# Kernel tuning notes

Measured on AMD Instinct MI355X. Metric: run time of the kernel, lower is better.

The kernel has to match this reference:

```python
import jax, jax.numpy as jnp
import numpy as np

V, N, K, D = 100000, 20000, 32, 128
NEG = -1e9  # masked logit value


def setup_inputs() -> dict:
    key = jax.random.key(0)
    ks = jax.random.split(key, 8)
    return {
        "nodes": jax.random.randint(ks[0], (N,), 0, V),
        "neigh_idx": jax.random.randint(ks[1], (N, K), 0, V),
        "degrees": jax.random.randint(ks[2], (N,), 0, K + 1),
        "u2e": jax.random.normal(ks[3], (V, D), dtype=jnp.float32),
        "W1": jax.random.normal(ks[4], (2 * D, D), dtype=jnp.float32) * 0.05,
        "b1": jnp.zeros((D,), jnp.float32),
        "W2": jax.random.normal(ks[5], (D, D), dtype=jnp.float32) * 0.05,
        "b2": jnp.zeros((D,), jnp.float32),
        "W3": jax.random.normal(ks[6], (D, 1), dtype=jnp.float32) * 0.05,
        "b3": jnp.zeros((1,), jnp.float32),
    }


def reference(nodes, neigh_idx, degrees, u2e, W1, b1, W2, b2, W3, b3):
    self_feats = u2e[nodes]                      # [N, D]
    e_u = u2e[neigh_idx]                         # [N, K, D] ragged gather (padded)
    # Attention MLP: cat(neighbor, self) -> relu -> relu -> scalar logit
    x = jnp.concatenate([e_u, jnp.broadcast_to(self_feats[:, None, :], (e_u.shape[0], K, D))], axis=-1)  # [N, K, 2D]
    h = jax.nn.relu(x @ W1 + b1)                 # [N, K, D]
    h = jax.nn.relu(h @ W2 + b2)                 # [N, K, D]
    logits = (h @ W3 + b3)[..., 0]               # [N, K]
    mask = jnp.arange(K)[None, :] < degrees[:, None]
    att = jax.nn.softmax(jnp.where(mask, logits, NEG), axis=-1)  # softmax over neighbors
    agg = jnp.einsum("nk,nkd->nd", att, e_u)     # attention-weighted neighbor sum
    out = jnp.where(degrees[:, None] > 0, (agg + self_feats) * 0.5, self_feats)
    return out
```

## Files before the change

kernel.cpp:

```cpp
#include <hip/hip_runtime.h>
#include <hip/hip_bf16.h>

#define KK 32
#define DD 128
#define NEGV (-1e9f)
#define SE 136
#define PREP_BLKS 2048

typedef __attribute__((ext_vector_type(8))) short bf16x8;
typedef __attribute__((ext_vector_type(4))) float f32x4;

__device__ __forceinline__ unsigned short f2bf(float f) {
    union { float f; unsigned u; } v; v.f = f;
    unsigned r = v.u + 0x7fffu + ((v.u >> 16) & 1u);
    return (unsigned short)(r >> 16);
}
__device__ __forceinline__ float bf2f(unsigned short h) {
    union { unsigned u; float f; } v; v.u = ((unsigned)h) << 16;
    return v.f;
}
__device__ __forceinline__ unsigned pk2(float x, float y) {
    union { __hip_bfloat162 h; unsigned u; } c;
    c.h = __float22bfloat162_rn(float2{x, y});
    return c.u;
}

__global__ __launch_bounds__(256) void prep_kernel(
    const float* __restrict__ u2e, const float* __restrict__ W1, const float* __restrict__ W2,
    unsigned short* __restrict__ u2e_bf, unsigned short* __restrict__ W1t,
    unsigned short* __restrict__ W2t, const int u2e_blocks, const long Vd)
{
    const int b = blockIdx.x;
    if (b < u2e_blocks) {
        const long stride = (long)u2e_blocks * 256 * 8;
        for (long i = ((long)b * 256 + threadIdx.x) * 8; i < Vd; i += stride) {
            const float4 v0 = *(const float4*)(u2e + i);
            const float4 v1 = *(const float4*)(u2e + i + 4);
            uint4 p;
            p.x = pk2(v0.x, v0.y); p.y = pk2(v0.z, v0.w);
            p.z = pk2(v1.x, v1.y); p.w = pk2(v1.z, v1.w);
            *(uint4*)(u2e_bf + i) = p;
        }
    } else {
        const int id = (b - u2e_blocks) * 256 + threadIdx.x;
        if (id < 256 * 128) {
            const int n = id >> 8, k = id & 255;
            W1t[id] = f2bf(W1[k * DD + n]);
        } else {
            const int j = id - 256 * 128;
            const int n = j >> 7, k = j & 127;
            W2t[j] = f2bf(W2[k * DD + n]);
        }
    }
}

template<bool BF>
__global__ __launch_bounds__(256, 2) void ppagg_mfma(
    const int* __restrict__ nodes, const int* __restrict__ neigh,
    const int* __restrict__ degrees, const float* __restrict__ u2e,
    const unsigned short* __restrict__ u2e_bf,
    const unsigned short* __restrict__ W1t, const unsigned short* __restrict__ W2t,
    const float* __restrict__ b1, const float* __restrict__ b2,
    const float* __restrict__ W3, const float* __restrict__ b3,
    float* __restrict__ out, const int Nn)
{
    __shared__ __align__(16) unsigned short s_A[128 * SE];
    __shared__ __align__(16) unsigned short s_B[128 * SE];
    __shared__ __align__(16) unsigned short s_x8[8 * DD];
    __shared__ float s_selfc[8 * 128];
    __shared__ float s_part[4][128];

    const int tid  = threadIdx.x;
    const int w    = tid >> 6;
    const int lane = tid & 63;
    const int ln   = lane & 15;
    const int q    = lane >> 4;

    const int nb = blockIdx.x * 8;
    const int r  = tid & 127;
    const int h  = tid >> 7;

    int idxA, idxB, vA, vB;
    {
        int ng0 = nb + (r >> 5);       if (ng0 >= Nn) ng0 = Nn - 1;
        int ng1 = nb + 4 + (r >> 5);   if (ng1 >= Nn) ng1 = Nn - 1;
        idxA = neigh[ng0 * KK + (r & 31)];
        idxB = neigh[ng1 * KK + (r & 31)];
        vA = (r & 31) < degrees[ng0];
        vB = (r & 31) < degrees[ng1];
    }

    auto stage = [&](unsigned short* buf, int idx, int v) {
        unsigned short* dst = buf + r * SE + h * 64;
        if (BF && v) {
            const uint4* src = (const uint4*)(u2e_bf + (long)idx * DD + h * 64);
            #pragma unroll
            for (int c = 0; c < 8; ++c) *(uint4*)(dst + c * 8) = src[c];
        } else if (!BF && v) {
            const float4* src = (const float4*)(u2e + (long)idx * DD + h * 64);
            #pragma unroll
            for (int c8 = 0; c8 < 8; ++c8) {
                const float4 v0 = src[c8 * 2];
                const float4 v1 = src[c8 * 2 + 1];
                uint4 p;
                p.x = pk2(v0.x, v0.y); p.y = pk2(v0.z, v0.w);
                p.z = pk2(v1.x, v1.y); p.w = pk2(v1.z, v1.w);
                *(uint4*)(dst + c8 * 8) = p;
            }
        } else {
            const uint4 z = {0u, 0u, 0u, 0u};
            #pragma unroll
            for (int c = 0; c < 8; ++c) *(uint4*)(dst + c * 8) = z;
        }
    };

    stage(s_A, idxA, vA);

    {
        int gn = nb + (tid >> 5); if (gn >= Nn) gn = Nn - 1;
        const int g = tid >> 5, p = tid & 31;
        const float4 v = *(const float4*)(u2e + (long)nodes[gn] * DD + p * 4);
        *(unsigned*)(s_x8 + g * DD + p * 4)     = pk2(v.x, v.y);
        *(unsigned*)(s_x8 + g * DD + p * 4 + 2) = pk2(v.z, v.w);
    }

    float2 self0, self1;
    {
        int n0 = nb + w;       if (n0 >= Nn) n0 = Nn - 1;
        int n1 = nb + 4 + w;   if (n1 >= Nn) n1 = Nn - 1;
        self0 = *(const float2*)(u2e + (long)nodes[n0] * DD + lane * 2);
        self1 = *(const float2*)(u2e + (long)nodes[n1] * DD + lane * 2);
    }

    bf16x8 b1f[4][2], b2f[4][2];
    float b1c[2], b2c[2], w3c[2];
    const int c0 = w * 32 + ln;
    const int c1 = c0 + 16;
    #pragma unroll
    for (int kk = 0; kk < 4; ++kk) {
        b1f[kk][0] = *(const bf16x8*)(W1t + c0 * 256 + kk * 32 + q * 8);
        b1f[kk][1] = *(const bf16x8*)(W1t + c1 * 256 + kk * 32 + q * 8);
        b2f[kk][0] = *(const bf16x8*)(W2t + c0 * 128 + kk * 32 + q * 8);
        b2f[kk][1] = *(const bf16x8*)(W2t + c1 * 128 + kk * 32 + q * 8);
    }
    b1c[0] = b1[c0]; b1c[1] = b1[c1];
    b2c[0] = b2[c0]; b2c[1] = b2[c1];
    w3c[0] = W3[c0]; w3c[1] = W3[c1];
    const float b3v = b3[0];

    __syncthreads();

    {
        f32x4 a0 = (f32x4){0.f,0.f,0.f,0.f}, a1 = (f32x4){0.f,0.f,0.f,0.f};
        #pragma unroll
        for (int kk = 0; kk < 4; ++kk) {
            const bf16x8 av = *(const bf16x8*)(s_x8 + (ln & 7) * DD + kk * 32 + q * 8);
            const bf16x8 w0 = *(const bf16x8*)(W1t + c0 * 256 + 128 + kk * 32 + q * 8);
            const bf16x8 w1 = *(const bf16x8*)(W1t + c1 * 256 + 128 + kk * 32 + q * 8);
            a0 = __builtin_amdgcn_mfma_f32_16x16x32_bf16(av, w0, a0, 0, 0, 0);
            a1 = __builtin_amdgcn_mfma_f32_16x16x32_bf16(av, w1, a1, 0, 0, 0);
        }
        if (q < 2) {
            #pragma unroll
            for (int rr = 0; rr < 4; ++rr) {
                s_selfc[(q * 4 + rr) * 128 + c0] = a0[rr] + b1c[0];
                s_selfc[(q * 4 + rr) * 128 + c1] = a1[rr] + b1c[1];
            }
        }
    }
    __syncthreads();

    #pragma unroll
    for (int it = 0; it < 2; ++it) {
        unsigned short* E = it ? s_B : s_A;
        unsigned short* H = it ? s_A : s_B;
        const int gbase = nb + it * 4;
        const float2 selfv = it ? self1 : self0;

        if (it == 1) __syncthreads();

        f32x4 acc[8][2];
        #pragma unroll
        for (int mt = 0; mt < 8; ++mt) {
            acc[mt][0] = (f32x4){0.f, 0.f, 0.f, 0.f};
            acc[mt][1] = (f32x4){0.f, 0.f, 0.f, 0.f};
        }
        #pragma unroll
        for (int kk = 0; kk < 4; ++kk) {
            bf16x8 a[8];
            #pragma unroll
            for (int mt = 0; mt < 8; ++mt)
                a[mt] = *(const bf16x8*)(E + (mt * 16 + ln) * SE + kk * 32 + q * 8);
            #pragma unroll
            for (int mt = 0; mt < 8; ++mt) {
                acc[mt][0] = __builtin_amdgcn_mfma_f32_16x16x32_bf16(a[mt], b1f[kk][0], acc[mt][0], 0, 0, 0);
                acc[mt][1] = __builtin_amdgcn_mfma_f32_16x16x32_bf16(a[mt], b1f[kk][1], acc[mt][1], 0, 0, 0);
            }
        }
        #pragma unroll
        for (int mt = 0; mt < 8; ++mt) {
            const float sc0 = s_selfc[(it * 4 + (mt >> 1)) * 128 + c0];
            const float sc1 = s_selfc[(it * 4 + (mt >> 1)) * 128 + c1];
            #pragma unroll
            for (int rr = 0; rr < 4; rr += 2) {
                const int row = mt * 16 + q * 4 + rr;
                const unsigned p0 = pk2(fmaxf(acc[mt][0][rr]     + sc0, 0.f),
                                        fmaxf(acc[mt][0][rr + 1] + sc0, 0.f));
                const unsigned p1v = pk2(fmaxf(acc[mt][1][rr]     + sc1, 0.f),
                                         fmaxf(acc[mt][1][rr + 1] + sc1, 0.f));
                H[row * SE + c0]       = (unsigned short)(p0 & 0xffffu);
                H[(row + 1) * SE + c0] = (unsigned short)(p0 >> 16);
                H[row * SE + c1]       = (unsigned short)(p1v & 0xffffu);
                H[(row + 1) * SE + c1] = (unsigned short)(p1v >> 16);
            }
        }
        __syncthreads();

        f32x4 acc2[8][2];
        #pragma unroll
        for (int mt = 0; mt < 8; ++mt) {
            acc2[mt][0] = (f32x4){0.f, 0.f, 0.f, 0.f};
            acc2[mt][1] = (f32x4){0.f, 0.f, 0.f, 0.f};
        }
        #pragma unroll
        for (int kk = 0; kk < 4; ++kk) {
            bf16x8 a[8];
            #pragma unroll
            for (int mt = 0; mt < 8; ++mt)
                a[mt] = *(const bf16x8*)(H + (mt * 16 + ln) * SE + kk * 32 + q * 8);
            #pragma unroll
            for (int mt = 0; mt < 8; ++mt) {
                acc2[mt][0] = __builtin_amdgcn_mfma_f32_16x16x32_bf16(a[mt], b2f[kk][0], acc2[mt][0], 0, 0, 0);
                acc2[mt][1] = __builtin_amdgcn_mfma_f32_16x16x32_bf16(a[mt], b2f[kk][1], acc2[mt][1], 0, 0, 0);
            }
        }
        #pragma unroll
        for (int mt = 0; mt < 8; ++mt) {
            float p[4];
            #pragma unroll
            for (int rr = 0; rr < 4; ++rr) {
                const float h0 = fmaxf(acc2[mt][0][rr] + b2c[0], 0.f);
                const float h1v = fmaxf(acc2[mt][1][rr] + b2c[1], 0.f);
                p[rr] = fmaf(h0, w3c[0], h1v * w3c[1]);
            }
            #pragma unroll
            for (int off = 1; off < 16; off <<= 1) {
                #pragma unroll
                for (int rr = 0; rr < 4; ++rr) p[rr] += __shfl_xor(p[rr], off);
            }
            if (ln == 0) {
                const int row0 = mt * 16 + q * 4;
                #pragma unroll
                for (int rr = 0; rr < 4; ++rr) s_part[w][row0 + rr] = p[rr];
            }
        }
        __syncthreads();

        if (it == 0) stage(s_B, idxB, vB);

        {
            const int ng  = gbase + w;
            const int ngc = (ng < Nn) ? ng : Nn - 1;
            const int deg = degrees[ngc];
            const int krow = lane & 31;
            const int rb = w * KK;
            const float logit = s_part[0][rb + krow] + s_part[1][rb + krow]
                              + s_part[2][rb + krow] + s_part[3][rb + krow] + b3v;
            const float ml = (krow < deg) ? logit : NEGV;
            float mx = ml;
            #pragma unroll
            for (int off = 16; off > 0; off >>= 1) mx = fmaxf(mx, __shfl_xor(mx, off));
            const float e = __expf(ml - mx);
            float ssum = e;
            #pragma unroll
            for (int off = 16; off > 0; off >>= 1) ssum += __shfl_xor(ssum, off);
            const float att = e / ssum;

            const int degw = (ng < Nn) ? deg : 0;
            float ax = 0.f, ay = 0.f;
            for (int k = 0; k < degw; ++k) {
                const float a = __shfl(att, k, 32);
                const unsigned pe = *(const unsigned*)(E + (rb + k) * SE + lane * 2);
                ax = fmaf(a, bf2f((unsigned short)(pe & 0xffffu)), ax);
                ay = fmaf(a, bf2f((unsigned short)(pe >> 16)), ay);
            }
            if (ng < Nn) {
                float2 o;
                o.x = (degw > 0) ? 0.5f * (ax + selfv.x) : selfv.x;
                o.y = (degw > 0) ? 0.5f * (ay + selfv.y) : selfv.y;
                *(float2*)(out + (long)ng * DD + lane * 2) = o;
            }
        }
    }
}

extern "C" void kernel_launch(void* const* d_in, const int* in_sizes, int n_in,
                              void* d_out, int out_size, void* d_ws, size_t ws_size,
                              hipStream_t stream) {
    const int*   nodes   = (const int*)d_in[0];
    const int*   neigh   = (const int*)d_in[1];
    const int*   degrees = (const int*)d_in[2];
    const float* u2e     = (const float*)d_in[3];
    const float* W1      = (const float*)d_in[4];
    const float* b1      = (const float*)d_in[5];
    const float* W2      = (const float*)d_in[6];
    const float* b2      = (const float*)d_in[7];
    const float* W3      = (const float*)d_in[8];
    const float* b3      = (const float*)d_in[9];
    float* out = (float*)d_out;

    const int  Nn = in_sizes[0];
    const long Vd = (long)in_sizes[3];

    unsigned short* W1t = (unsigned short*)d_ws;
    unsigned short* W2t = W1t + 256 * 128;
    unsigned short* u2e_bf = W2t + 128 * 128;

    const size_t need_bf = (size_t)(256 * 128 + 128 * 128) * 2 + (size_t)Vd * 2;
    const bool use_bf = (ws_size >= need_bf) && (Vd % 8 == 0);
    const int u2e_blocks = use_bf ? PREP_BLKS : 0;

    prep_kernel<<<u2e_blocks + 192, 256, 0, stream>>>(u2e, W1, W2, u2e_bf, W1t, W2t,
                                                      u2e_blocks, Vd);

    const int grid = (Nn + 7) / 8;
    if (use_bf)
        ppagg_mfma<true><<<grid, 256, 0, stream>>>(nodes, neigh, degrees, u2e, u2e_bf,
                                                   W1t, W2t, b1, b2, W3, b3, out, Nn);
    else
        ppagg_mfma<false><<<grid, 256, 0, stream>>>(nodes, neigh, degrees, u2e, nullptr,
                                                    W1t, W2t, b1, b2, W3, b3, out, Nn);
}
```

Measured before the change: 226.5 us.

## Swap MFMA operand order to transpose accumulators and vectorize epilogues

```diff
diff --git a/kernel.cpp b/kernel.cpp
--- a/kernel.cpp
+++ b/kernel.cpp
@@ -67,8 +67,10 @@
     __shared__ __align__(16) unsigned short s_A[128 * SE];
     __shared__ __align__(16) unsigned short s_B[128 * SE];
     __shared__ __align__(16) unsigned short s_x8[8 * DD];
-    __shared__ float s_selfc[8 * 128];
+    __shared__ __align__(16) float s_selfc[8 * 128];
+    __shared__ __align__(16) float s_b2w3[256];
     __shared__ float s_part[4][128];
+    __shared__ float s_att[128];
 
     const int tid  = threadIdx.x;
     const int w    = tid >> 6;
@@ -122,6 +124,7 @@
         const float4 v = *(const float4*)(u2e + (long)nodes[gn] * DD + p * 4);
         *(unsigned*)(s_x8 + g * DD + p * 4)     = pk2(v.x, v.y);
         *(unsigned*)(s_x8 + g * DD + p * 4 + 2) = pk2(v.z, v.w);
+        s_b2w3[tid] = (tid < 128) ? b2[tid] : W3[tid - 128];
     }
 
     float2 self0, self1;
@@ -133,7 +136,7 @@
     }
 
     bf16x8 b1f[4][2], b2f[4][2];
-    float b1c[2], b2c[2], w3c[2];
+    float b1c[2];
     const int c0 = w * 32 + ln;
     const int c1 = c0 + 16;
     #pragma unroll
@@ -144,8 +147,6 @@
         b2f[kk][1] = *(const bf16x8*)(W2t + c1 * 128 + kk * 32 + q * 8);
     }
     b1c[0] = b1[c0]; b1c[1] = b1[c1];
-    b2c[0] = b2[c0]; b2c[1] = b2[c1];
-    w3c[0] = W3[c0]; w3c[1] = W3[c1];
     const float b3v = b3[0];
 
     __syncthreads();
@@ -193,25 +194,23 @@
                 a[mt] = *(const bf16x8*)(E + (mt * 16 + ln) * SE + kk * 32 + q * 8);
             #pragma unroll
             for (int mt = 0; mt < 8; ++mt) {
-                acc[mt][0] = __builtin_amdgcn_mfma_f32_16x16x32_bf16(a[mt], b1f[kk][0], acc[mt][0], 0, 0, 0);
-                acc[mt][1] = __builtin_amdgcn_mfma_f32_16x16x32_bf16(a[mt], b1f[kk][1], acc[mt][1], 0, 0, 0);
+                acc[mt][0] = __builtin_amdgcn_mfma_f32_16x16x32_bf16(b1f[kk][0], a[mt], acc[mt][0], 0, 0, 0);
+                acc[mt][1] = __builtin_amdgcn_mfma_f32_16x16x32_bf16(b1f[kk][1], a[mt], acc[mt][1], 0, 0, 0);
             }
         }
         #pragma unroll
         for (int mt = 0; mt < 8; ++mt) {
-            const float sc0 = s_selfc[(it * 4 + (mt >> 1)) * 128 + c0];
-            const float sc1 = s_selfc[(it * 4 + (mt >> 1)) * 128 + c1];
-            #pragma unroll
-            for (int rr = 0; rr < 4; rr += 2) {
-                const int row = mt * 16 + q * 4 + rr;
-                const unsigned p0 = pk2(fmaxf(acc[mt][0][rr]     + sc0, 0.f),
-                                        fmaxf(acc[mt][0][rr + 1] + sc0, 0.f));
-                const unsigned p1v = pk2(fmaxf(acc[mt][1][rr]     + sc1, 0.f),
-                                         fmaxf(acc[mt][1][rr + 1] + sc1, 0.f));
-                H[row * SE + c0]       = (unsigned short)(p0 & 0xffffu);
-                H[(row + 1) * SE + c0] = (unsigned short)(p0 >> 16);
-                H[row * SE + c1]       = (unsigned short)(p1v & 0xffffu);
-                H[(row + 1) * SE + c1] = (unsigned short)(p1v >> 16);
+            const int node = it * 4 + (mt >> 1);
+            #pragma unroll
+            for (int nt = 0; nt < 2; ++nt) {
+                const int nb4 = w * 32 + nt * 16 + q * 4;
+                const f32x4 sc = *(const f32x4*)(s_selfc + node * 128 + nb4);
+                uint2 pw;
+                pw.x = pk2(fmaxf(acc[mt][nt][0] + sc[0], 0.f),
+                           fmaxf(acc[mt][nt][1] + sc[1], 0.f));
+                pw.y = pk2(fmaxf(acc[mt][nt][2] + sc[2], 0.f),
+                           fmaxf(acc[mt][nt][3] + sc[3], 0.f));
+                *(uint2*)(H + (mt * 16 + ln) * SE + nb4) = pw;
             }
         }
         __syncthreads();
@@ -230,43 +229,39 @@
                 a[mt] = *(const bf16x8*)(H + (mt * 16 + ln) * SE + kk * 32 + q * 8);
             #pragma unroll
             for (int mt = 0; mt < 8; ++mt) {
-                acc2[mt][0] = __builtin_amdgcn_mfma_f32_16x16x32_bf16(a[mt], b2f[kk][0], acc2[mt][0], 0, 0, 0);
-                acc2[mt][1] = __builtin_amdgcn_mfma_f32_16x16x32_bf16(a[mt], b2f[kk][1], acc2[mt][1], 0, 0, 0);
-            }
-        }
-        #pragma unroll
-        for (int mt = 0; mt < 8; ++mt) {
-            float p[4];
-            #pragma unroll
-            for (int rr = 0; rr < 4; ++rr) {
-                const float h0 = fmaxf(acc2[mt][0][rr] + b2c[0], 0.f);
-                const float h1v = fmaxf(acc2[mt][1][rr] + b2c[1], 0.f);
-                p[rr] = fmaf(h0, w3c[0], h1v * w3c[1]);
-            }
-            #pragma unroll
-            for (int off = 1; off < 16; off <<= 1) {
+                acc2[mt][0] = __builtin_amdgcn_mfma_f32_16x16x32_bf16(b2f[kk][0], a[mt], acc2[mt][0], 0, 0, 0);
+                acc2[mt][1] = __builtin_amdgcn_mfma_f32_16x16x32_bf16(b2f[kk][1], a[mt], acc2[mt][1], 0, 0, 0);
+            }
+        }
+        {
+            const f32x4 b2v0 = *(const f32x4*)(s_b2w3 + w * 32 + q * 4);
+            const f32x4 b2v1 = *(const f32x4*)(s_b2w3 + w * 32 + 16 + q * 4);
+            const f32x4 w3v0 = *(const f32x4*)(s_b2w3 + 128 + w * 32 + q * 4);
+            const f32x4 w3v1 = *(const f32x4*)(s_b2w3 + 128 + w * 32 + 16 + q * 4);
+            #pragma unroll
+            for (int mt = 0; mt < 8; ++mt) {
+                float pl = 0.f;
                 #pragma unroll
-                for (int rr = 0; rr < 4; ++rr) p[rr] += __shfl_xor(p[rr], off);
-            }
-            if (ln == 0) {
-                const int row0 = mt * 16 + q * 4;
-                #pragma unroll
-                for (int rr = 0; rr < 4; ++rr) s_part[w][row0 + rr] = p[rr];
+                for (int rr = 0; rr < 4; ++rr) {
+                    pl = fmaf(fmaxf(acc2[mt][0][rr] + b2v0[rr], 0.f), w3v0[rr], pl);
+                    pl = fmaf(fmaxf(acc2[mt][1][rr] + b2v1[rr], 0.f), w3v1[rr], pl);
+                }
+                pl += __shfl_xor(pl, 16);
+                pl += __shfl_xor(pl, 32);
+                if (lane < 16) s_part[w][mt * 16 + ln] = pl;
             }
         }
         __syncthreads();
 
         if (it == 0) stage(s_B, idxB, vB);
 
-        {
-            const int ng  = gbase + w;
-            const int ngc = (ng < Nn) ? ng : Nn - 1;
-            const int deg = degrees[ngc];
-            const int krow = lane & 31;
-            const int rb = w * KK;
-            const float logit = s_part[0][rb + krow] + s_part[1][rb + krow]
-                              + s_part[2][rb + krow] + s_part[3][rb + krow] + b3v;
-            const float ml = (krow < deg) ? logit : NEGV;
+        if (tid < 128) {
+            const int row = tid;
+            const float logit = s_part[0][row] + s_part[1][row] + s_part[2][row] + s_part[3][row] + b3v;
+            int ng = gbase + (row >> 5);
+            if (ng >= Nn) ng = Nn - 1;
+            const int deg = degrees[ng];
+            const float ml = ((row & 31) < deg) ? logit : NEGV;
             float mx = ml;
             #pragma unroll
             for (int off = 16; off > 0; off >>= 1) mx = fmaxf(mx, __shfl_xor(mx, off));
@@ -274,13 +269,17 @@
             float ssum = e;
             #pragma unroll
             for (int off = 16; off > 0; off >>= 1) ssum += __shfl_xor(ssum, off);
-            const float att = e / ssum;
-
-            const int degw = (ng < Nn) ? deg : 0;
+            s_att[row] = e / ssum;
+        }
+        __syncthreads();
+
+        {
+            const int ng = gbase + w;
+            const int degw = (ng < Nn) ? degrees[ng] : 0;
             float ax = 0.f, ay = 0.f;
             for (int k = 0; k < degw; ++k) {
-                const float a = __shfl(att, k, 32);
-                const unsigned pe = *(const unsigned*)(E + (rb + k) * SE + lane * 2);
+                const float a = s_att[w * KK + k];
+                const unsigned pe = *(const unsigned*)(E + (w * KK + k) * SE + lane * 2);
                 ax = fmaf(a, bf2f((unsigned short)(pe & 0xffffu)), ax);
                 ay = fmaf(a, bf2f((unsigned short)(pe >> 16)), ay);
             }
```

Result: faster. 204.2 us (-9.8%).
